# Kernel optimization log

Measured on AMD Instinct MI355X. Metric: run time of the kernel, lower is better.

## Reference

```python
import jax, jax.numpy as jnp
import numpy as np


def _pair_indices(n_beads):
    # Replicates the torch loop ordering: all pairs at offset 1, then offset 2, ...
    i_list, j_list = [], []
    for off in range(1, n_beads):
        i = np.arange(n_beads - off)
        i_list.append(i)
        j_list.append(i + off)
    return np.concatenate(i_list), np.concatenate(j_list)


def setup_inputs() -> dict:
    key = jax.random.key(0)
    data = jax.random.normal(key, (4096, 128, 3), dtype=jnp.float32)
    return {"data": data}


def _features(data):
    n = data.shape[1]
    i_idx, j_idx = _pair_indices(n)  # static numpy index arrays

    # All pairwise distances, ordered by bead offset (matches torch loop order)
    dvec = data[:, j_idx, :] - data[:, i_idx, :]          # [B, P, 3]
    distances = jnp.linalg.norm(dvec, axis=2)             # [B, P]

    # Adjacent bond vectors: x[j+1] - x[j]
    adj = data[:, 1:, :] - data[:, :-1, :]                # [B, n-1, 3]

    # Planar angles over consecutive bond-vector pairs
    a0, a1 = adj[:, : n - 2, :], adj[:, 1 : n - 1, :]
    angles = jnp.arccos(
        jnp.sum(a0 * a1, axis=2)
        / jnp.linalg.norm(a0, axis=2)
        / jnp.linalg.norm(a1, axis=2)
    )                                                     # [B, n-2]

    # Dihedrals
    cpa = jnp.cross(a0, a1, axis=2)                       # [B, n-2, 3]
    plane = jnp.cross(cpa[:, 1 : n - 2, :], adj[:, 1 : n - 2, :], axis=2)  # [B, n-3, 3]
    c0, c1 = cpa[:, : n - 3, :], cpa[:, 1 : n - 2, :]
    nc0 = jnp.linalg.norm(c0, axis=2)
    dihedral_cos = jnp.sum(c0 * c1, axis=2) / nc0 / jnp.linalg.norm(c1, axis=2)
    p0 = plane[:, : n - 3, :]
    dihedral_sin = jnp.sum(c0 * p0, axis=2) / nc0 / jnp.linalg.norm(p0, axis=2)

    return jnp.concatenate([distances, angles, dihedral_cos, dihedral_sin], axis=1)


def reference(data):
    return _features(data)
```

## Files before the change

kernel.cpp:

```cpp
#include <hip/hip_runtime.h>
#include <math.h>

constexpr int NB    = 128;
constexpr int NPAIR = NB * (NB - 1) / 2;
constexpr int NANG  = NB - 2;
constexpr int NDIH  = NB - 3;
constexpr int ROW   = NPAIR + NANG + 2 * NDIH;

__global__ __launch_bounds__(1024, 8) void protein_feat_kernel(
        const float* __restrict__ data, float* __restrict__ out) {
    __shared__ float4 s4[NB];
    const int b  = blockIdx.x;
    const int t  = threadIdx.x;
    const int tb = t & 127;
    const int g  = t >> 7;
    const float* src = data + (size_t)b * (NB * 3);

    if (t < NB)
        s4[t] = make_float4(src[3 * t], src[3 * t + 1], src[3 * t + 2], 0.0f);
    __syncthreads();

    float* orow = out + (size_t)b * ROW;

    float px[4], py[4], pz[4];
    #pragma unroll
    for (int k = 0; k < 4; ++k) {
        int idx = tb - k; if (idx < 0) idx = 0;
        float4 v = s4[idx];
        px[k] = v.x; py[k] = v.y; pz[k] = v.z;
    }

    #pragma unroll
    for (int m = 0; m < 4; ++m) {
        const int off = 1 + 4 * g + 32 * m;
        const int len = NB - off;
        const int bk0 = (off - 1) * (2 * NB - off) / 2;
        const int bk1 = bk0 + len;
        const int bk2 = bk1 + len - 1;
        const int bk3 = bk2 + len - 2;
        if (tb < len) {
            float4 pj = s4[tb + off];
            float dx, dy, dz, d;
            dx = pj.x - px[0]; dy = pj.y - py[0]; dz = pj.z - pz[0];
            d = __builtin_amdgcn_sqrtf(dx*dx + dy*dy + dz*dz);
            orow[bk0 + tb] = d;
            dx = pj.x - px[1]; dy = pj.y - py[1]; dz = pj.z - pz[1];
            d = __builtin_amdgcn_sqrtf(dx*dx + dy*dy + dz*dz);
            if (tb >= 1) orow[bk1 + tb - 1] = d;
            dx = pj.x - px[2]; dy = pj.y - py[2]; dz = pj.z - pz[2];
            d = __builtin_amdgcn_sqrtf(dx*dx + dy*dy + dz*dz);
            if (tb >= 2) orow[bk2 + tb - 2] = d;
            dx = pj.x - px[3]; dy = pj.y - py[3]; dz = pj.z - pz[3];
            d = __builtin_amdgcn_sqrtf(dx*dx + dy*dy + dz*dz);
            if (tb >= 3) orow[bk3 + tb - 3] = d;
        }
    }

    const int v = t;
    if (v < NANG + 2 * NDIH) {
        if (v < NANG) {
            int a = v;
            float4 p0 = s4[a], p1 = s4[a + 1], p2 = s4[a + 2];
            float a0x = p1.x - p0.x, a0y = p1.y - p0.y, a0z = p1.z - p0.z;
            float a1x = p2.x - p1.x, a1y = p2.y - p1.y, a1z = p2.z - p1.z;
            float d  = a0x * a1x + a0y * a1y + a0z * a1z;
            float r0 = rsqrtf(a0x * a0x + a0y * a0y + a0z * a0z);
            float r1 = rsqrtf(a1x * a1x + a1y * a1y + a1z * a1z);
            float c  = d * r0 * r1;
            c = fminf(1.0f, fmaxf(-1.0f, c));
            orow[NPAIR + a] = acosf(c);
        } else {
            int a = (v < NANG + NDIH) ? (v - NANG) : (v - NANG - NDIH);
            float4 p0 = s4[a], p1 = s4[a + 1], p2 = s4[a + 2], p3 = s4[a + 3];
            float e0x = p1.x - p0.x, e0y = p1.y - p0.y, e0z = p1.z - p0.z;
            float e1x = p2.x - p1.x, e1y = p2.y - p1.y, e1z = p2.z - p1.z;
            float e2x = p3.x - p2.x, e2y = p3.y - p2.y, e2z = p3.z - p2.z;
            float c0x = e0y * e1z - e0z * e1y;
            float c0y = e0z * e1x - e0x * e1z;
            float c0z = e0x * e1y - e0y * e1x;
            float c1x = e1y * e2z - e1z * e2y;
            float c1y = e1z * e2x - e1x * e2z;
            float c1z = e1x * e2y - e1y * e2x;
            float rn0 = rsqrtf(c0x * c0x + c0y * c0y + c0z * c0z);
            if (v < NANG + NDIH) {
                float d   = c0x * c1x + c0y * c1y + c0z * c1z;
                float rn1 = rsqrtf(c1x * c1x + c1y * c1y + c1z * c1z);
                orow[NPAIR + NANG + a] = d * rn0 * rn1;
            } else {
                float qx = c1y * e1z - c1z * e1y;
                float qy = c1z * e1x - c1x * e1z;
                float qz = c1x * e1y - c1y * e1x;
                float d  = c0x * qx + c0y * qy + c0z * qz;
                float rp = rsqrtf(qx * qx + qy * qy + qz * qz);
                orow[NPAIR + NANG + NDIH + a] = d * rn0 * rp;
            }
        }
    }
}

extern "C" void kernel_launch(void* const* d_in, const int* in_sizes, int n_in,
                              void* d_out, int out_size, void* d_ws, size_t ws_size,
                              hipStream_t stream) {
    const float* data = (const float*)d_in[0];
    float* out = (float*)d_out;
    const int batch = in_sizes[0] / (NB * 3);
    protein_feat_kernel<<<batch, 1024, 0, stream>>>(data, out);
}
```

Measured before the change: 31.34 us.

## Pair offsets with complementary wraparound so all threads compute distances

Replaces the per-thread four-source distance scheme with a cyclic mapping. Each thread takes offset off and index (tb+off) mod 128. When the index wraps, the result goes into the complementary offset's segment (NB-off), so every lane in every group stays active with no tail predication. Each group now covers 8 offsets with a single source point. This removes divergence and idle lanes, at the cost of scattered store addresses at the wrap point and some modular index arithmetic.

```diff
diff --git a/kernel.cpp b/kernel.cpp
--- a/kernel.cpp
+++ b/kernel.cpp
@@ -22,47 +22,30 @@
 
     float* orow = out + (size_t)b * ROW;
 
-    float px[4], py[4], pz[4];
-    #pragma unroll
-    for (int k = 0; k < 4; ++k) {
-        int idx = tb - k; if (idx < 0) idx = 0;
-        float4 v = s4[idx];
-        px[k] = v.x; py[k] = v.y; pz[k] = v.z;
-    }
+    const float4 p0 = s4[tb];
 
-    #pragma unroll
-    for (int m = 0; m < 4; ++m) {
-        const int off = 1 + 4 * g + 32 * m;
-        const int len = NB - off;
-        const int bk0 = (off - 1) * (2 * NB - off) / 2;
-        const int bk1 = bk0 + len;
-        const int bk2 = bk1 + len - 1;
-        const int bk3 = bk2 + len - 2;
-        if (tb < len) {
-            float4 pj = s4[tb + off];
-            float dx, dy, dz, d;
-            dx = pj.x - px[0]; dy = pj.y - py[0]; dz = pj.z - pz[0];
-            d = __builtin_amdgcn_sqrtf(dx*dx + dy*dy + dz*dz);
-            orow[bk0 + tb] = d;
-            dx = pj.x - px[1]; dy = pj.y - py[1]; dz = pj.z - pz[1];
-            d = __builtin_amdgcn_sqrtf(dx*dx + dy*dy + dz*dz);
-            if (tb >= 1) orow[bk1 + tb - 1] = d;
-            dx = pj.x - px[2]; dy = pj.y - py[2]; dz = pj.z - pz[2];
-            d = __builtin_amdgcn_sqrtf(dx*dx + dy*dy + dz*dz);
-            if (tb >= 2) orow[bk2 + tb - 2] = d;
-            dx = pj.x - px[3]; dy = pj.y - py[3]; dz = pj.z - pz[3];
-            d = __builtin_amdgcn_sqrtf(dx*dx + dy*dy + dz*dz);
-            if (tb >= 3) orow[bk3 + tb - 3] = d;
-        }
+    #pragma unroll 2
+    for (int m = 0; m < 8; ++m) {
+        const int off = 8 * g + 1 + m;
+        const int r2  = NB - off;
+        const int c1  = (off - 1) * (2 * NB - off) / 2;
+        const int c2  = (r2 - 1) * (2 * NB - r2) / 2 - r2;
+        float4 pj = s4[(tb + off) & (NB - 1)];
+        float dx = pj.x - p0.x;
+        float dy = pj.y - p0.y;
+        float dz = pj.z - p0.z;
+        float d  = __builtin_amdgcn_sqrtf(dx * dx + dy * dy + dz * dz);
+        const int base = (tb + off < NB) ? c1 : c2;
+        orow[base + tb] = d;
     }
 
     const int v = t;
     if (v < NANG + 2 * NDIH) {
         if (v < NANG) {
             int a = v;
-            float4 p0 = s4[a], p1 = s4[a + 1], p2 = s4[a + 2];
-            float a0x = p1.x - p0.x, a0y = p1.y - p0.y, a0z = p1.z - p0.z;
-            float a1x = p2.x - p1.x, a1y = p2.y - p1.y, a1z = p2.z - p1.z;
+            float4 q0 = s4[a], q1 = s4[a + 1], q2 = s4[a + 2];
+            float a0x = q1.x - q0.x, a0y = q1.y - q0.y, a0z = q1.z - q0.z;
+            float a1x = q2.x - q1.x, a1y = q2.y - q1.y, a1z = q2.z - q1.z;
             float d  = a0x * a1x + a0y * a1y + a0z * a1z;
             float r0 = rsqrtf(a0x * a0x + a0y * a0y + a0z * a0z);
             float r1 = rsqrtf(a1x * a1x + a1y * a1y + a1z * a1z);
@@ -71,10 +54,10 @@
             orow[NPAIR + a] = acosf(c);
         } else {
             int a = (v < NANG + NDIH) ? (v - NANG) : (v - NANG - NDIH);
-            float4 p0 = s4[a], p1 = s4[a + 1], p2 = s4[a + 2], p3 = s4[a + 3];
-            float e0x = p1.x - p0.x, e0y = p1.y - p0.y, e0z = p1.z - p0.z;
-            float e1x = p2.x - p1.x, e1y = p2.y - p1.y, e1z = p2.z - p1.z;
-            float e2x = p3.x - p2.x, e2y = p3.y - p2.y, e2z = p3.z - p2.z;
+            float4 q0 = s4[a], q1 = s4[a + 1], q2 = s4[a + 2], q3 = s4[a + 3];
+            float e0x = q1.x - q0.x, e0y = q1.y - q0.y, e0z = q1.z - q0.z;
+            float e1x = q2.x - q1.x, e1y = q2.y - q1.y, e1z = q2.z - q1.z;
+            float e2x = q3.x - q2.x, e2y = q3.y - q2.y, e2z = q3.z - q2.z;
             float c0x = e0y * e1z - e0z * e1y;
             float c0y = e0z * e1x - e0x * e1z;
             float c0z = e0x * e1y - e0y * e1x;
```

Result: slower. 33.43 us (+6.7%).

## Process eight proteins per block with double-buffered register prefetch

Applied to the files above, without the earlier changes.

Each block now loops over eight batch entries instead of one. Before computing the current protein, it loads the next protein's coordinates into registers and then writes them to a second shared-memory buffer. This is meant to amortise block launch cost and hide global-load latency behind compute. In exchange the grid shrinks to 512 blocks of 1024 threads, which may underfill the GPU. It also assumes the batch is divisible by eight.

```diff
diff --git a/kernel.cpp b/kernel.cpp
--- a/kernel.cpp
+++ b/kernel.cpp
@@ -6,95 +6,114 @@
 constexpr int NANG  = NB - 2;
 constexpr int NDIH  = NB - 3;
 constexpr int ROW   = NPAIR + NANG + 2 * NDIH;
+constexpr int PPB   = 8;
 
 __global__ __launch_bounds__(1024, 8) void protein_feat_kernel(
         const float* __restrict__ data, float* __restrict__ out) {
-    __shared__ float4 s4[NB];
-    const int b  = blockIdx.x;
+    __shared__ float4 s4[2][NB];
     const int t  = threadIdx.x;
     const int tb = t & 127;
     const int g  = t >> 7;
-    const float* src = data + (size_t)b * (NB * 3);
+    const int p0 = blockIdx.x * PPB;
 
-    if (t < NB)
-        s4[t] = make_float4(src[3 * t], src[3 * t + 1], src[3 * t + 2], 0.0f);
+    if (t < NB) {
+        const float* s = data + (size_t)p0 * (NB * 3) + 3 * t;
+        s4[0][t] = make_float4(s[0], s[1], s[2], 0.0f);
+    }
     __syncthreads();
 
-    float* orow = out + (size_t)b * ROW;
+    int cur = 0;
+    for (int it = 0; it < PPB; ++it) {
+        const int p = p0 + it;
 
-    float px[4], py[4], pz[4];
-    #pragma unroll
-    for (int k = 0; k < 4; ++k) {
-        int idx = tb - k; if (idx < 0) idx = 0;
-        float4 v = s4[idx];
-        px[k] = v.x; py[k] = v.y; pz[k] = v.z;
-    }
+        float nx = 0.f, ny = 0.f, nz = 0.f;
+        const bool pf = (t < NB) && (it + 1 < PPB);
+        if (pf) {
+            const float* s = data + (size_t)(p + 1) * (NB * 3) + 3 * t;
+            nx = s[0]; ny = s[1]; nz = s[2];
+        }
 
-    #pragma unroll
-    for (int m = 0; m < 4; ++m) {
-        const int off = 1 + 4 * g + 32 * m;
-        const int len = NB - off;
-        const int bk0 = (off - 1) * (2 * NB - off) / 2;
-        const int bk1 = bk0 + len;
-        const int bk2 = bk1 + len - 1;
-        const int bk3 = bk2 + len - 2;
-        if (tb < len) {
-            float4 pj = s4[tb + off];
-            float dx, dy, dz, d;
-            dx = pj.x - px[0]; dy = pj.y - py[0]; dz = pj.z - pz[0];
-            d = __builtin_amdgcn_sqrtf(dx*dx + dy*dy + dz*dz);
-            orow[bk0 + tb] = d;
-            dx = pj.x - px[1]; dy = pj.y - py[1]; dz = pj.z - pz[1];
-            d = __builtin_amdgcn_sqrtf(dx*dx + dy*dy + dz*dz);
-            if (tb >= 1) orow[bk1 + tb - 1] = d;
-            dx = pj.x - px[2]; dy = pj.y - py[2]; dz = pj.z - pz[2];
-            d = __builtin_amdgcn_sqrtf(dx*dx + dy*dy + dz*dz);
-            if (tb >= 2) orow[bk2 + tb - 2] = d;
-            dx = pj.x - px[3]; dy = pj.y - py[3]; dz = pj.z - pz[3];
-            d = __builtin_amdgcn_sqrtf(dx*dx + dy*dy + dz*dz);
-            if (tb >= 3) orow[bk3 + tb - 3] = d;
+        float* orow = out + (size_t)p * ROW;
+
+        float px[4], py[4], pz[4];
+        #pragma unroll
+        for (int k = 0; k < 4; ++k) {
+            int idx = tb - k; if (idx < 0) idx = 0;
+            float4 v = s4[cur][idx];
+            px[k] = v.x; py[k] = v.y; pz[k] = v.z;
         }
-    }
 
-    const int v = t;
-    if (v < NANG + 2 * NDIH) {
-        if (v < NANG) {
-            int a = v;
-            float4 p0 = s4[a], p1 = s4[a + 1], p2 = s4[a + 2];
-            float a0x = p1.x - p0.x, a0y = p1.y - p0.y, a0z = p1.z - p0.z;
-            float a1x = p2.x - p1.x, a1y = p2.y - p1.y, a1z = p2.z - p1.z;
-            float d  = a0x * a1x + a0y * a1y + a0z * a1z;
-            float r0 = rsqrtf(a0x * a0x + a0y * a0y + a0z * a0z);
-            float r1 = rsqrtf(a1x * a1x + a1y * a1y + a1z * a1z);
-            float c  = d * r0 * r1;
-            c = fminf(1.0f, fmaxf(-1.0f, c));
-            orow[NPAIR + a] = acosf(c);
-        } else {
-            int a = (v < NANG + NDIH) ? (v - NANG) : (v - NANG - NDIH);
-            float4 p0 = s4[a], p1 = s4[a + 1], p2 = s4[a + 2], p3 = s4[a + 3];
-            float e0x = p1.x - p0.x, e0y = p1.y - p0.y, e0z = p1.z - p0.z;
-            float e1x = p2.x - p1.x, e1y = p2.y - p1.y, e1z = p2.z - p1.z;
-            float e2x = p3.x - p2.x, e2y = p3.y - p2.y, e2z = p3.z - p2.z;
-            float c0x = e0y * e1z - e0z * e1y;
-            float c0y = e0z * e1x - e0x * e1z;
-            float c0z = e0x * e1y - e0y * e1x;
-            float c1x = e1y * e2z - e1z * e2y;
-            float c1y = e1z * e2x - e1x * e2z;
-            float c1z = e1x * e2y - e1y * e2x;
-            float rn0 = rsqrtf(c0x * c0x + c0y * c0y + c0z * c0z);
-            if (v < NANG + NDIH) {
-                float d   = c0x * c1x + c0y * c1y + c0z * c1z;
-                float rn1 = rsqrtf(c1x * c1x + c1y * c1y + c1z * c1z);
-                orow[NPAIR + NANG + a] = d * rn0 * rn1;
-            } else {
-                float qx = c1y * e1z - c1z * e1y;
-                float qy = c1z * e1x - c1x * e1z;
-                float qz = c1x * e1y - c1y * e1x;
-                float d  = c0x * qx + c0y * qy + c0z * qz;
-                float rp = rsqrtf(qx * qx + qy * qy + qz * qz);
-                orow[NPAIR + NANG + NDIH + a] = d * rn0 * rp;
+        #pragma unroll
+        for (int m = 0; m < 4; ++m) {
+            const int off = 1 + 4 * g + 32 * m;
+            const int len = NB - off;
+            const int bk0 = (off - 1) * (2 * NB - off) / 2;
+            const int bk1 = bk0 + len;
+            const int bk2 = bk1 + len - 1;
+            const int bk3 = bk2 + len - 2;
+            if (tb < len) {
+                float4 pj = s4[cur][tb + off];
+                float dx, dy, dz, d;
+                dx = pj.x - px[0]; dy = pj.y - py[0]; dz = pj.z - pz[0];
+                d = __builtin_amdgcn_sqrtf(dx*dx + dy*dy + dz*dz);
+                orow[bk0 + tb] = d;
+                dx = pj.x - px[1]; dy = pj.y - py[1]; dz = pj.z - pz[1];
+                d = __builtin_amdgcn_sqrtf(dx*dx + dy*dy + dz*dz);
+                if (tb >= 1) orow[bk1 + tb - 1] = d;
+                dx = pj.x - px[2]; dy = pj.y - py[2]; dz = pj.z - pz[2];
+                d = __builtin_amdgcn_sqrtf(dx*dx + dy*dy + dz*dz);
+                if (tb >= 2) orow[bk2 + tb - 2] = d;
+                dx = pj.x - px[3]; dy = pj.y - py[3]; dz = pj.z - pz[3];
+                d = __builtin_amdgcn_sqrtf(dx*dx + dy*dy + dz*dz);
+                if (tb >= 3) orow[bk3 + tb - 3] = d;
             }
         }
+
+        if (t < NANG + 2 * NDIH) {
+            const int v = t;
+            if (v < NANG) {
+                int a = v;
+                float4 q0 = s4[cur][a], q1 = s4[cur][a+1], q2 = s4[cur][a+2];
+                float a0x = q1.x - q0.x, a0y = q1.y - q0.y, a0z = q1.z - q0.z;
+                float a1x = q2.x - q1.x, a1y = q2.y - q1.y, a1z = q2.z - q1.z;
+                float d  = a0x * a1x + a0y * a1y + a0z * a1z;
+                float r0 = rsqrtf(a0x * a0x + a0y * a0y + a0z * a0z);
+                float r1 = rsqrtf(a1x * a1x + a1y * a1y + a1z * a1z);
+                float c  = d * r0 * r1;
+                c = fminf(1.0f, fmaxf(-1.0f, c));
+                orow[NPAIR + a] = acosf(c);
+            } else {
+                int a = (v < NANG + NDIH) ? (v - NANG) : (v - NANG - NDIH);
+                float4 q0 = s4[cur][a],   q1 = s4[cur][a+1];
+                float4 q2 = s4[cur][a+2], q3 = s4[cur][a+3];
+                float e0x = q1.x - q0.x, e0y = q1.y - q0.y, e0z = q1.z - q0.z;
+                float e1x = q2.x - q1.x, e1y = q2.y - q1.y, e1z = q2.z - q1.z;
+                float e2x = q3.x - q2.x, e2y = q3.y - q2.y, e2z = q3.z - q2.z;
+                float c0x = e0y * e1z - e0z * e1y;
+                float c0y = e0z * e1x - e0x * e1z;
+                float c0z = e0x * e1y - e0y * e1x;
+                float c1x = e1y * e2z - e1z * e2y;
+                float c1y = e1z * e2x - e1x * e2z;
+                float c1z = e1x * e2y - e1y * e2x;
+                float rn0 = rsqrtf(c0x * c0x + c0y * c0y + c0z * c0z);
+                if (v < NANG + NDIH) {
+                    float d   = c0x * c1x + c0y * c1y + c0z * c1z;
+                    float rn1 = rsqrtf(c1x * c1x + c1y * c1y + c1z * c1z);
+                    orow[NPAIR + NANG + a] = d * rn0 * rn1;
+                } else {
+                    float qx = c1y * e1z - c1z * e1y;
+                    float qy = c1z * e1x - c1x * e1z;
+                    float qz = c1x * e1y - c1y * e1x;
+                    float d  = c0x * qx + c0y * qy + c0z * qz;
+                    float rp = rsqrtf(qx * qx + qy * qy + qz * qz);
+                    orow[NPAIR + NANG + NDIH + a] = d * rn0 * rp;
+                }
+            }
+        }
+
+        if (pf) s4[cur ^ 1][t] = make_float4(nx, ny, nz, 0.0f);
+        __syncthreads();
+        cur ^= 1;
     }
 }
 
@@ -104,5 +123,5 @@
     const float* data = (const float*)d_in[0];
     float* out = (float*)d_out;
     const int batch = in_sizes[0] / (NB * 3);
-    protein_feat_kernel<<<batch, 1024, 0, stream>>>(data, out);
+    protein_feat_kernel<<<batch / PPB, 1024, 0, stream>>>(data, out);
 }
```

Result: slower. 53.57 us (+70.9%).
